# Kernel tuning notes

Measured on AMD Instinct MI355X. Metric: run time of the kernel, lower is better.

## Reference

```python
import jax, jax.numpy as jnp
import numpy as np

EPS = 1e-9
NUM_CLASSES = 10


def setup_inputs() -> dict:
    key = jax.random.key(0)
    k1, k2, k3, k4 = jax.random.split(key, 4)
    B, N, D = 1024, 16384, 512
    bound = 1.0 / (D ** 0.5)
    return {
        "x": jax.random.normal(k1, (B, D), dtype=jnp.float32),
        "ex_feats": jax.random.normal(k2, (N, D), dtype=jnp.float32),
        "ex_labels": jax.random.randint(k3, (N,), 0, NUM_CLASSES),
        "w_unconstrained": jax.random.uniform(k4, (D,), dtype=jnp.float32, minval=-bound, maxval=bound),
        "gamma_unconstrained": jnp.asarray(1.0, dtype=jnp.float32),
        "beta_unconstrained": jnp.asarray(1.0, dtype=jnp.float32),
    }


def reference(x, ex_feats, ex_labels, w_unconstrained, gamma_unconstrained, beta_unconstrained):
    # Constrained parameters
    beta = jax.nn.softplus(beta_unconstrained) + EPS      # scalar
    gamma = jax.nn.softplus(gamma_unconstrained) + EPS    # scalar
    w = jax.nn.softmax(w_unconstrained) + EPS             # (D,), positive, ~sums to 1

    # Weighted squared distance via quadratic (GEMM) expansion:
    # d[b,n] = sum_k w_k * (x[b,k] - e[n,k])^2
    #        = (x^2 @ w)[b] + (e^2 @ w)[n] - 2 * ((x*w) @ e^T)[b,n]
    x2w = (x * x) @ w                                     # (B,)
    e2w = (ex_feats * ex_feats) @ w                       # (N,)
    cross = (x * w[None, :]) @ ex_feats.T                 # (B, N) GEMM
    d = x2w[:, None] + e2w[None, :] - 2.0 * cross         # (B, N)

    sim = jnp.exp(-beta * d)                              # (B, N)

    # Scatter-add sim by class label -> class_sum (B, C).
    # With small C this is a dense GEMM against a one-hot matrix.
    onehot = jax.nn.one_hot(ex_labels, NUM_CLASSES, dtype=sim.dtype)  # (N, C)
    class_sum = sim @ onehot                              # (B, C)

    logits = gamma * jnp.log(class_sum + EPS)
    return logits
```

## Files before the change

### kernel.cpp

```cpp
#include <hip/hip_runtime.h>
#include <hip/hip_bf16.h>
#include <cstdint>


typedef __attribute__((ext_vector_type(4))) float f32x4;
typedef __attribute__((ext_vector_type(8))) __bf16 bf16x8;
typedef __attribute__((ext_vector_type(4))) _Float16 half4;
typedef __attribute__((ext_vector_type(4))) unsigned int u32x4;

#define DDIM 512
#define NC 10
#define NCP 16
#define NECH 64
#define EPSF 1e-9f

__device__ inline float softplus(float x) {
  return (x > 20.0f) ? x : log1pf(__expf(x));
}

__device__ inline unsigned cvtpk(float lo, float hi) {
  unsigned r;
  asm("v_cvt_pk_bf16_f32 %0, %1, %2" : "=v"(r) : "v"(lo), "v"(hi));
  return r;
}

__global__ __launch_bounds__(1024, 4) void gemm_mega(
    const float* __restrict__ x, const float* __restrict__ ex,
    const int* __restrict__ labels, const float* __restrict__ wu,
    const float* __restrict__ bu, float* __restrict__ part) {
  __shared__ __attribute__((aligned(16))) unsigned short smem[2 * 16384];
  __shared__ float wlds[512];
  __shared__ float sm[16];
  __shared__ float e2l[256];
  __shared__ float x2l[256];
  __shared__ int lab[256];
  const int tid = threadIdx.x, lane = tid & 63, wid = tid >> 6;

  const int orig = blockIdx.x;
  const int xcd = orig & 7;
  const int local = orig >> 3;
  const int be = xcd * 8 + (local >> 2);
  const int bb = local & 3;

  if (tid < 256) lab[tid] = labels[be * 256 + tid];

  if (tid < 512) {
    float v = wu[tid];
    float m = v;
    #pragma unroll
    for (int o = 32; o > 0; o >>= 1) m = fmaxf(m, __shfl_xor(m, o, 64));
    if (lane == 0) sm[wid] = m;
    __syncthreads();
    float mm = sm[0];
    #pragma unroll
    for (int i = 1; i < 8; ++i) mm = fmaxf(mm, sm[i]);
    float e = __expf(v - mm);
    float s = e;
    #pragma unroll
    for (int o = 32; o > 0; o >>= 1) s += __shfl_xor(s, o, 64);
    if (lane == 0) sm[8 + wid] = s;
    __syncthreads();
    float ss = 0.f;
    #pragma unroll
    for (int i = 0; i < 8; ++i) ss += sm[8 + i];
    wlds[tid] = e / ss + EPSF;
  } else {
    __syncthreads();
    __syncthreads();
  }
  __syncthreads();

  const int srow = tid >> 2;
  const int kc = (tid & 3) ^ ((srow >> 1) & 3);
  const float* eP = ex + (size_t)(be * 256 + srow) * DDIM + kc * 8;
  const float* xP = x + (size_t)(bb * 256 + srow) * DDIM + kc * 8;
  const int dE = tid * 8;
  const int dX = 8192 + tid * 8;

  float e2a = 0.f, x2a = 0.f;

  const int WE = (wid >> 2) * 64;
  const int WB = (wid & 3) * 64;
  int eoff[4], xoff[4];
  {
    const int ch = lane >> 4;
    #pragma unroll
    for (int f = 0; f < 4; ++f) {
      int er = WE + f * 16 + (lane & 15);
      eoff[f] = er * 64 + ((ch ^ ((er >> 1) & 3)) * 16);
      int xr = WB + f * 16 + (lane & 15);
      xoff[f] = 16384 + xr * 64 + ((ch ^ ((xr >> 1) & 3)) * 16);
    }
  }

  float4 sEa, sEb, sXa, sXb;

#define ISSUE(KT) do {                                                  \
    const float* p0 = eP + (KT) * 32;                                   \
    const float* p1 = xP + (KT) * 32;                                   \
    sEa = *(const float4*)p0; sEb = *(const float4*)(p0 + 4);           \
    sXa = *(const float4*)p1; sXb = *(const float4*)(p1 + 4);           \
  } while (0)

#define CVTSTORE(KT, BUFS) do {                                         \
    const float4 w0 = *(const float4*)&wlds[(KT) * 32 + kc * 8];        \
    const float4 w1 = *(const float4*)&wlds[(KT) * 32 + kc * 8 + 4];    \
    u32x4 pk;                                                           \
    pk[0] = cvtpk(sEa.x, sEa.y); pk[1] = cvtpk(sEa.z, sEa.w);           \
    pk[2] = cvtpk(sEb.x, sEb.y); pk[3] = cvtpk(sEb.z, sEb.w);           \
    e2a += sEa.x*sEa.x*w0.x + sEa.y*sEa.y*w0.y                          \
         + sEa.z*sEa.z*w0.z + sEa.w*sEa.w*w0.w                          \
         + sEb.x*sEb.x*w1.x + sEb.y*sEb.y*w1.y                          \
         + sEb.z*sEb.z*w1.z + sEb.w*sEb.w*w1.w;                         \
    *(u32x4*)&smem[(BUFS) + dE] = pk;                                   \
    float a0 = sXa.x*w0.x, a1 = sXa.y*w0.y, a2 = sXa.z*w0.z,            \
          a3 = sXa.w*w0.w, a4 = sXb.x*w1.x, a5 = sXb.y*w1.y,            \
          a6 = sXb.z*w1.z, a7 = sXb.w*w1.w;                             \
    pk[0] = cvtpk(a0, a1); pk[1] = cvtpk(a2, a3);                       \
    pk[2] = cvtpk(a4, a5); pk[3] = cvtpk(a6, a7);                       \
    x2a += a0*sXa.x + a1*sXa.y + a2*sXa.z + a3*sXa.w                    \
         + a4*sXb.x + a5*sXb.y + a6*sXb.z + a7*sXb.w;                   \
    *(u32x4*)&smem[(BUFS) + dX] = pk;                                   \
  } while (0)

  ISSUE(0);
  CVTSTORE(0, 0);
  __syncthreads();

  f32x4 acc[4][4] = {};
  for (int kt = 0; kt < 16; ++kt) {
    const int cur = kt & 1;
    if (kt < 15) ISSUE(kt + 1);
    const char* base = (const char*)smem + cur * 32768;
    bf16x8 ef[4], xf[4];
    #pragma unroll
    for (int f = 0; f < 4; ++f) {
      ef[f] = *(const bf16x8*)(base + eoff[f]);
      xf[f] = *(const bf16x8*)(base + xoff[f]);
    }
    #pragma unroll
    for (int fe = 0; fe < 4; ++fe)
      #pragma unroll
      for (int fb = 0; fb < 4; ++fb)
        acc[fe][fb] = __builtin_amdgcn_mfma_f32_16x16x32_bf16(ef[fe], xf[fb], acc[fe][fb], 0, 0, 0);
    if (kt < 15) CVTSTORE(kt + 1, (cur ^ 1) * 16384);
    __syncthreads();
  }
#undef ISSUE
#undef CVTSTORE

  e2a += __shfl_xor(e2a, 1, 64); e2a += __shfl_xor(e2a, 2, 64);
  x2a += __shfl_xor(x2a, 1, 64); x2a += __shfl_xor(x2a, 2, 64);
  if ((tid & 3) == 0) {
    e2l[srow] = e2a;
    x2l[srow] = x2a;
  }
  __syncthreads();

  const float beta = softplus(bu[0]) + EPSF;
  const int rb = (lane >> 4) * 4;
  const int col = lane & 15;
  float e2v[4][4];
  #pragma unroll
  for (int fe = 0; fe < 4; ++fe)
    #pragma unroll
    for (int r = 0; r < 4; ++r)
      e2v[fe][r] = e2l[WE + fe * 16 + rb + r];
  half4 oh[4];
  #pragma unroll
  for (int fe = 0; fe < 4; ++fe)
    #pragma unroll
    for (int i = 0; i < 4; ++i)
      oh[fe][i] = (lab[WE + fe * 16 + rb + i] == col) ? (_Float16)1.0f : (_Float16)0.0f;

  f32x4 csv[4];
  #pragma unroll
  for (int fb = 0; fb < 4; ++fb) {
    const float xv = x2l[WB + fb * 16 + col];
    f32x4 cs = {0.f, 0.f, 0.f, 0.f};
    #pragma unroll
    for (int fe = 0; fe < 4; ++fe) {
      half4 sa;
      #pragma unroll
      for (int r = 0; r < 4; ++r)
        sa[r] = (_Float16)__expf(-beta * (xv + e2v[fe][r] - 2.0f * acc[fe][fb][r]));
      cs = __builtin_amdgcn_mfma_f32_16x16x16f16(sa, oh[fe], cs, 0, 0, 0);
    }
    csv[fb] = cs;
  }

  float* red = (float*)smem;
  const int quad = WE >> 6;
  #pragma unroll
  for (int fb = 0; fb < 4; ++fb)
    #pragma unroll
    for (int r = 0; r < 4; ++r)
      red[((quad * 256 + (WB + fb * 16 + rb + r)) << 4) | col] = csv[fb][r];
  __syncthreads();

  {
    const int o = tid * 4;
    const int rl = o >> 4;
    const int c0 = o & 12;
    float4 v0 = *(const float4*)&red[(rl << 4) | c0];
    float4 v1 = *(const float4*)&red[((256 + rl) << 4) | c0];
    float4 v2 = *(const float4*)&red[((512 + rl) << 4) | c0];
    float4 v3 = *(const float4*)&red[((768 + rl) << 4) | c0];
    float4 r0 = {v0.x + v1.x + v2.x + v3.x, v0.y + v1.y + v2.y + v3.y,
                 v0.z + v1.z + v2.z + v3.z, v0.w + v1.w + v2.w + v3.w};
    *(float4*)&part[(((size_t)(bb * 256 + rl)) * NECH + be) * NCP + c0] = r0;
  }
}

__global__ __launch_bounds__(256) void reduce_logits(
    const float* __restrict__ part, const float* __restrict__ gu,
    float* __restrict__ out) {
  const int lane = threadIdx.x & 63, wd = threadIdx.x >> 6;
  const int b = blockIdx.x * 4 + wd;
  const int cl = lane & 15, ch0 = lane >> 4;
  const float* p = part + (size_t)b * NECH * NCP;
  float v = 0.f;
  #pragma unroll
  for (int k = 0; k < 16; ++k)
    v += p[(ch0 + 4 * k) * NCP + cl];
  v += __shfl_xor(v, 16, 64);
  v += __shfl_xor(v, 32, 64);
  if (lane < NC) {
    const float gamma = softplus(gu[0]) + EPSF;
    out[b * NC + lane] = gamma * logf(v + EPSF);
  }
}

extern "C" void kernel_launch(void* const* d_in, const int* in_sizes, int n_in,
                              void* d_out, int out_size, void* d_ws, size_t ws_size,
                              hipStream_t stream) {
  const float* x  = (const float*)d_in[0];
  const float* ex = (const float*)d_in[1];
  const int* labels = (const int*)d_in[2];
  const float* wu = (const float*)d_in[3];
  const float* gu = (const float*)d_in[4];
  const float* bu = (const float*)d_in[5];
  float* out = (float*)d_out;
  const int B = in_sizes[0] / DDIM;
  const int N = in_sizes[2];

  float* part = (float*)d_ws;
  const size_t need = (size_t)B * NECH * NCP * 4;
  if (ws_size < need) return;

  gemm_mega<<<(N / 256) * (B / 256), 1024, 0, stream>>>(x, ex, labels, wu, bu, part);
  reduce_logits<<<B / 4, 256, 0, stream>>>(part, gu, out);
}
```

Measured before the change: 38.08 us.

## Precompute bf16 weighted x in prep kernel and stream it via async LDS loads

```diff
diff --git a/kernel.cpp b/kernel.cpp
--- a/kernel.cpp
+++ b/kernel.cpp
@@ -14,6 +14,13 @@
 #define NECH 64
 #define EPSF 1e-9f
 
+typedef const __attribute__((address_space(1))) void* gas_ptr;
+typedef __attribute__((address_space(3))) void* las_ptr;
+
+__device__ inline void async16(const void* g, void* l) {
+  __builtin_amdgcn_global_load_lds((gas_ptr)g, (las_ptr)l, 16, 0, 0);
+}
+
 __device__ inline float softplus(float x) {
   return (x > 20.0f) ? x : log1pf(__expf(x));
 }
@@ -24,63 +31,94 @@
   return r;
 }
 
-__global__ __launch_bounds__(1024, 4) void gemm_mega(
-    const float* __restrict__ x, const float* __restrict__ ex,
-    const int* __restrict__ labels, const float* __restrict__ wu,
-    const float* __restrict__ bu, float* __restrict__ part) {
-  __shared__ __attribute__((aligned(16))) unsigned short smem[2 * 16384];
+__global__ __launch_bounds__(512) void prep_x(
+    const float* __restrict__ x, const float* __restrict__ wu,
+    float* __restrict__ wbuf, unsigned short* __restrict__ xbf,
+    float* __restrict__ x2w) {
+  __shared__ float sm[16];
+  const int tid = threadIdx.x, lane = tid & 63, wid = tid >> 6;
+
+  float v = wu[tid];
+  float m = v;
+  #pragma unroll
+  for (int o = 32; o > 0; o >>= 1) m = fmaxf(m, __shfl_xor(m, o, 64));
+  if (lane == 0) sm[wid] = m;
+  __syncthreads();
+  float mm = sm[0];
+  #pragma unroll
+  for (int i = 1; i < 8; ++i) mm = fmaxf(mm, sm[i]);
+  float e = __expf(v - mm);
+  float s = e;
+  #pragma unroll
+  for (int o = 32; o > 0; o >>= 1) s += __shfl_xor(s, o, 64);
+  if (lane == 0) sm[8 + wid] = s;
+  __syncthreads();
+  float ss = 0.f;
+  #pragma unroll
+  for (int i = 0; i < 8; ++i) ss += sm[8 + i];
+  const float wv = e / ss + EPSF;
+  wbuf[tid] = wv;
+
   __shared__ float wlds[512];
-  __shared__ float sm[16];
+  wlds[tid] = wv;
+  __syncthreads();
+  const float4 wa = *(const float4*)&wlds[lane * 8];
+  const float4 wb = *(const float4*)&wlds[lane * 8 + 4];
+
+  const size_t row = (size_t)blockIdx.x * 8 + wid;
+  const float* p = x + row * DDIM + lane * 8;
+  float4 va = *(const float4*)(p);
+  float4 vb = *(const float4*)(p + 4);
+  float a0 = va.x * wa.x, a1 = va.y * wa.y, a2 = va.z * wa.z, a3 = va.w * wa.w;
+  float a4 = vb.x * wb.x, a5 = vb.y * wb.y, a6 = vb.z * wb.z, a7 = vb.w * wb.w;
+  float s2 = a0 * va.x + a1 * va.y + a2 * va.z + a3 * va.w
+           + a4 * vb.x + a5 * vb.y + a6 * vb.z + a7 * vb.w;
+  u32x4 pk;
+  pk[0] = cvtpk(a0, a1); pk[1] = cvtpk(a2, a3);
+  pk[2] = cvtpk(a4, a5); pk[3] = cvtpk(a6, a7);
+  *(u32x4*)(xbf + row * DDIM + lane * 8) = pk;
+  #pragma unroll
+  for (int o = 32; o > 0; o >>= 1) s2 += __shfl_xor(s2, o, 64);
+  if (lane == 0) x2w[row] = s2;
+}
+
+__global__ __launch_bounds__(512, 4) void gemm_mega(
+    const float* __restrict__ ex, const unsigned short* __restrict__ xbf,
+    const int* __restrict__ labels, const float* __restrict__ wbuf,
+    const float* __restrict__ x2w, const float* __restrict__ bu,
+    float* __restrict__ part) {
+  __shared__ __attribute__((aligned(16))) unsigned short smem[2 * 12288];
+  __shared__ float wlds[512];
   __shared__ float e2l[256];
-  __shared__ float x2l[256];
   __shared__ int lab[256];
   const int tid = threadIdx.x, lane = tid & 63, wid = tid >> 6;
 
   const int orig = blockIdx.x;
   const int xcd = orig & 7;
   const int local = orig >> 3;
-  const int be = xcd * 8 + (local >> 2);
-  const int bb = local & 3;
+  const int be = xcd * 8 + (local >> 3);
+  const int bb = local & 7;
 
   if (tid < 256) lab[tid] = labels[be * 256 + tid];
-
-  if (tid < 512) {
-    float v = wu[tid];
-    float m = v;
-    #pragma unroll
-    for (int o = 32; o > 0; o >>= 1) m = fmaxf(m, __shfl_xor(m, o, 64));
-    if (lane == 0) sm[wid] = m;
-    __syncthreads();
-    float mm = sm[0];
-    #pragma unroll
-    for (int i = 1; i < 8; ++i) mm = fmaxf(mm, sm[i]);
-    float e = __expf(v - mm);
-    float s = e;
-    #pragma unroll
-    for (int o = 32; o > 0; o >>= 1) s += __shfl_xor(s, o, 64);
-    if (lane == 0) sm[8 + wid] = s;
-    __syncthreads();
-    float ss = 0.f;
-    #pragma unroll
-    for (int i = 0; i < 8; ++i) ss += sm[8 + i];
-    wlds[tid] = e / ss + EPSF;
-  } else {
-    __syncthreads();
-    __syncthreads();
-  }
-  __syncthreads();
-
-  const int srow = tid >> 2;
-  const int kc = (tid & 3) ^ ((srow >> 1) & 3);
-  const float* eP = ex + (size_t)(be * 256 + srow) * DDIM + kc * 8;
-  const float* xP = x + (size_t)(bb * 256 + srow) * DDIM + kc * 8;
-  const int dE = tid * 8;
+  wlds[tid] = wbuf[tid];
+
+  const int erow = tid >> 1;
+  const int c0 = (tid & 1) * 2;
+  const int kc0 = c0 ^ ((erow >> 1) & 3);
+  const int kc1 = (c0 + 1) ^ ((erow >> 1) & 3);
+  const float* eP0 = ex + (size_t)(be * 256 + erow) * DDIM + kc0 * 8;
+  const float* eP1 = ex + (size_t)(be * 256 + erow) * DDIM + kc1 * 8;
+  const int dE0 = tid * 16, dE1 = tid * 16 + 8;
+
+  const int xrow = tid >> 2;
+  const int xkc = (tid & 3) ^ ((xrow >> 1) & 3);
+  const unsigned short* xP = xbf + (size_t)(bb * 128 + xrow) * DDIM + xkc * 8;
   const int dX = 8192 + tid * 8;
 
-  float e2a = 0.f, x2a = 0.f;
-
-  const int WE = (wid >> 2) * 64;
-  const int WB = (wid & 3) * 64;
+  float e2a = 0.f;
+
+  const int WE = (wid >> 1) * 64;
+  const int WB = (wid & 1) * 64;
   int eoff[4], xoff[4];
   {
     const int ch = lane >> 4;
@@ -93,18 +131,20 @@
     }
   }
 
-  float4 sEa, sEb, sXa, sXb;
+  float4 sEa, sEb, sEc, sEd;
 
 #define ISSUE(KT) do {                                                  \
-    const float* p0 = eP + (KT) * 32;                                   \
-    const float* p1 = xP + (KT) * 32;                                   \
+    const float* p0 = eP0 + (KT) * 32;                                  \
+    const float* p1 = eP1 + (KT) * 32;                                  \
     sEa = *(const float4*)p0; sEb = *(const float4*)(p0 + 4);           \
-    sXa = *(const float4*)p1; sXb = *(const float4*)(p1 + 4);           \
+    sEc = *(const float4*)p1; sEd = *(const float4*)(p1 + 4);           \
   } while (0)
 
 #define CVTSTORE(KT, BUFS) do {                                         \
-    const float4 w0 = *(const float4*)&wlds[(KT) * 32 + kc * 8];        \
-    const float4 w1 = *(const float4*)&wlds[(KT) * 32 + kc * 8 + 4];    \
+    const float4 w0 = *(const float4*)&wlds[(KT) * 32 + kc0 * 8];       \
+    const float4 w1 = *(const float4*)&wlds[(KT) * 32 + kc0 * 8 + 4];   \
+    const float4 w2 = *(const float4*)&wlds[(KT) * 32 + kc1 * 8];       \
+    const float4 w3 = *(const float4*)&wlds[(KT) * 32 + kc1 * 8 + 4];   \
     u32x4 pk;                                                           \
     pk[0] = cvtpk(sEa.x, sEa.y); pk[1] = cvtpk(sEa.z, sEa.w);           \
     pk[2] = cvtpk(sEb.x, sEb.y); pk[3] = cvtpk(sEb.z, sEb.w);           \
@@ -112,26 +152,32 @@
          + sEa.z*sEa.z*w0.z + sEa.w*sEa.w*w0.w                          \
          + sEb.x*sEb.x*w1.x + sEb.y*sEb.y*w1.y                          \
          + sEb.z*sEb.z*w1.z + sEb.w*sEb.w*w1.w;                         \
-    *(u32x4*)&smem[(BUFS) + dE] = pk;                                   \
-    float a0 = sXa.x*w0.x, a1 = sXa.y*w0.y, a2 = sXa.z*w0.z,            \
-          a3 = sXa.w*w0.w, a4 = sXb.x*w1.x, a5 = sXb.y*w1.y,            \
-          a6 = sXb.z*w1.z, a7 = sXb.w*w1.w;                             \
-    pk[0] = cvtpk(a0, a1); pk[1] = cvtpk(a2, a3);                       \
-    pk[2] = cvtpk(a4, a5); pk[3] = cvtpk(a6, a7);                       \
-    x2a += a0*sXa.x + a1*sXa.y + a2*sXa.z + a3*sXa.w                    \
-         + a4*sXb.x + a5*sXb.y + a6*sXb.z + a7*sXb.w;                   \
-    *(u32x4*)&smem[(BUFS) + dX] = pk;                                   \
+    *(u32x4*)&smem[(BUFS) + dE0] = pk;                                  \
+    pk[0] = cvtpk(sEc.x, sEc.y); pk[1] = cvtpk(sEc.z, sEc.w);           \
+    pk[2] = cvtpk(sEd.x, sEd.y); pk[3] = cvtpk(sEd.z, sEd.w);           \
+    e2a += sEc.x*sEc.x*w2.x + sEc.y*sEc.y*w2.y                          \
+         + sEc.z*sEc.z*w2.z + sEc.w*sEc.w*w2.w                          \
+         + sEd.x*sEd.x*w3.x + sEd.y*sEd.y*w3.y                          \
+         + sEd.z*sEd.z*w3.z + sEd.w*sEd.w*w3.w;                         \
+    *(u32x4*)&smem[(BUFS) + dE1] = pk;                                  \
   } while (0)
 
+  __syncthreads();
+
   ISSUE(0);
+  async16(xP, &smem[dX]);
   CVTSTORE(0, 0);
   __syncthreads();
 
   f32x4 acc[4][4] = {};
   for (int kt = 0; kt < 16; ++kt) {
     const int cur = kt & 1;
-    if (kt < 15) ISSUE(kt + 1);
-    const char* base = (const char*)smem + cur * 32768;
+    const int nb = (cur ^ 1) * 12288;
+    if (kt < 15) {
+      ISSUE(kt + 1);
+      async16(xP + (kt + 1) * 32, &smem[nb + dX]);
+    }
+    const char* base = (const char*)smem + cur * 24576;
     bf16x8 ef[4], xf[4];
     #pragma unroll
     for (int f = 0; f < 4; ++f) {
@@ -143,18 +189,14 @@
       #pragma unroll
       for (int fb = 0; fb < 4; ++fb)
         acc[fe][fb] = __builtin_amdgcn_mfma_f32_16x16x32_bf16(ef[fe], xf[fb], acc[fe][fb], 0, 0, 0);
-    if (kt < 15) CVTSTORE(kt + 1, (cur ^ 1) * 16384);
+    if (kt < 15) CVTSTORE(kt + 1, nb);
     __syncthreads();
   }
 #undef ISSUE
 #undef CVTSTORE
 
-  e2a += __shfl_xor(e2a, 1, 64); e2a += __shfl_xor(e2a, 2, 64);
-  x2a += __shfl_xor(x2a, 1, 64); x2a += __shfl_xor(x2a, 2, 64);
-  if ((tid & 3) == 0) {
-    e2l[srow] = e2a;
-    x2l[srow] = x2a;
-  }
+  e2a += __shfl_xor(e2a, 1, 64);
+  if ((tid & 1) == 0) e2l[erow] = e2a;
   __syncthreads();
 
   const float beta = softplus(bu[0]) + EPSF;
@@ -176,7 +218,7 @@
   f32x4 csv[4];
   #pragma unroll
   for (int fb = 0; fb < 4; ++fb) {
-    const float xv = x2l[WB + fb * 16 + col];
+    const float xv = x2w[bb * 128 + WB + fb * 16 + col];
     f32x4 cs = {0.f, 0.f, 0.f, 0.f};
     #pragma unroll
     for (int fe = 0; fe < 4; ++fe) {
@@ -195,20 +237,20 @@
   for (int fb = 0; fb < 4; ++fb)
     #pragma unroll
     for (int r = 0; r < 4; ++r)
-      red[((quad * 256 + (WB + fb * 16 + rb + r)) << 4) | col] = csv[fb][r];
+      red[((quad * 128 + (WB + fb * 16 + rb + r)) << 4) | col] = csv[fb][r];
   __syncthreads();
 
   {
     const int o = tid * 4;
     const int rl = o >> 4;
-    const int c0 = o & 12;
-    float4 v0 = *(const float4*)&red[(rl << 4) | c0];
-    float4 v1 = *(const float4*)&red[((256 + rl) << 4) | c0];
-    float4 v2 = *(const float4*)&red[((512 + rl) << 4) | c0];
-    float4 v3 = *(const float4*)&red[((768 + rl) << 4) | c0];
+    const int c0b = o & 12;
+    float4 v0 = *(const float4*)&red[(rl << 4) | c0b];
+    float4 v1 = *(const float4*)&red[((128 + rl) << 4) | c0b];
+    float4 v2 = *(const float4*)&red[((256 + rl) << 4) | c0b];
+    float4 v3 = *(const float4*)&red[((384 + rl) << 4) | c0b];
     float4 r0 = {v0.x + v1.x + v2.x + v3.x, v0.y + v1.y + v2.y + v3.y,
                  v0.z + v1.z + v2.z + v3.z, v0.w + v1.w + v2.w + v3.w};
-    *(float4*)&part[(((size_t)(bb * 256 + rl)) * NECH + be) * NCP + c0] = r0;
+    *(float4*)&part[(((size_t)(bb * 128 + rl)) * NECH + be) * NCP + c0b] = r0;
   }
 }
 
@@ -244,10 +286,20 @@
   const int B = in_sizes[0] / DDIM;
   const int N = in_sizes[2];
 
-  float* part = (float*)d_ws;
-  const size_t need = (size_t)B * NECH * NCP * 4;
+  char* ws = (char*)d_ws;
+  const size_t off_w    = 0;
+  const size_t off_x2w  = 4096;
+  const size_t off_xbf  = off_x2w + (size_t)B * 4;
+  const size_t off_part = off_xbf + (size_t)B * DDIM * 2;
+  const size_t need     = off_part + (size_t)B * NECH * NCP * 4;
   if (ws_size < need) return;
 
-  gemm_mega<<<(N / 256) * (B / 256), 1024, 0, stream>>>(x, ex, labels, wu, bu, part);
+  float* wbuf = (float*)(ws + off_w);
+  float* x2w  = (float*)(ws + off_x2w);
+  unsigned short* xbf = (unsigned short*)(ws + off_xbf);
+  float* part = (float*)(ws + off_part);
+
+  prep_x<<<B / 8, 512, 0, stream>>>(x, wu, wbuf, xbf, x2w);
+  gemm_mega<<<(N / 256) * (B / 128), 512, 0, stream>>>(ex, xbf, labels, wbuf, x2w, bu, part);
   reduce_logits<<<B / 4, 256, 0, stream>>>(part, gu, out);
 }
```

Result: slower. 53.74 us (+41.1%).
